# Optimization experiments

Measured on AMD Instinct MI355X. Metric: run time of the kernel, lower is better.

Reference implementation:

```python
import jax, jax.numpy as jnp
import numpy as np

CLIP_FRAMES = 16
CLIP_STRIDE = 8
D_CODE = 256
K_CODE = 8192
ENC_DIM = 128 * CLIP_FRAMES * 4 * 4  # 32768
EPS = 1e-5


def setup_inputs() -> dict:
    key = jax.random.key(0)
    ks = jax.random.split(key, 16)
    rn = lambda k, s, sc: (jax.random.normal(k, s, jnp.float32) * sc)
    inp = {}
    inp['x'] = jax.random.normal(ks[0], (4, 3, 64, 96, 96), jnp.float32)
    inp['conv1_w'] = rn(ks[1], (32, 3, 3, 3, 3), 0.1)
    inp['conv1_b'] = jnp.zeros((32,), jnp.float32)
    inp['bn1_g'] = jnp.ones((32,), jnp.float32)
    inp['bn1_b'] = jnp.zeros((32,), jnp.float32)
    inp['conv2_w'] = rn(ks[2], (64, 32, 3, 3, 3), 0.05)
    inp['conv2_b'] = jnp.zeros((64,), jnp.float32)
    inp['bn2_g'] = jnp.ones((64,), jnp.float32)
    inp['bn2_b'] = jnp.zeros((64,), jnp.float32)
    inp['conv3_w'] = rn(ks[3], (128, 64, 3, 3, 3), 0.04)
    inp['conv3_b'] = jnp.zeros((128,), jnp.float32)
    inp['bn3_g'] = jnp.ones((128,), jnp.float32)
    inp['bn3_b'] = jnp.zeros((128,), jnp.float32)
    inp['proj_w'] = rn(ks[4], (D_CODE, ENC_DIM), 0.005)
    inp['proj_b'] = jnp.zeros((D_CODE,), jnp.float32)
    inp['codebook'] = jax.random.uniform(ks[5], (K_CODE, D_CODE), jnp.float32, -1.0 / K_CODE, 1.0 / K_CODE)
    inp['gru_w_ih'] = rn(ks[6], (3 * D_CODE, D_CODE), 0.05)
    inp['gru_w_hh'] = rn(ks[7], (3 * D_CODE, D_CODE), 0.05)
    inp['gru_b_ih'] = jnp.zeros((3 * D_CODE,), jnp.float32)
    inp['gru_b_hh'] = jnp.zeros((3 * D_CODE,), jnp.float32)
    return inp


def _conv3d(x, w, b):
    y = jax.lax.conv_general_dilated(x, w, (1, 1, 1), ((1, 1), (1, 1), (1, 1)),
                                     dimension_numbers=('NCDHW', 'OIDHW', 'NCDHW'))
    return y + b[None, :, None, None, None]


def _bn(x, g, b):
    # training-mode BatchNorm3d: batch stats over (N,D,H,W), biased variance
    m = x.mean(axis=(0, 2, 3, 4), keepdims=True)
    v = ((x - m) ** 2).mean(axis=(0, 2, 3, 4), keepdims=True)
    return g[None, :, None, None, None] * (x - m) * jax.lax.rsqrt(v + EPS) + b[None, :, None, None, None]


def _maxpool(x):
    return jax.lax.reduce_window(x, -jnp.inf, jax.lax.max, (1, 1, 1, 2, 2), (1, 1, 1, 2, 2), 'VALID')


def _adaptive_avgpool(x):
    # [N,128,16,24,24] -> [N,128,16,4,4]; 24/4=6 exact window
    s = jax.lax.reduce_window(x, 0.0, jax.lax.add, (1, 1, 1, 6, 6), (1, 1, 1, 6, 6), 'VALID')
    return s / 36.0


def _gru(xs, w_ih, w_hh, b_ih, b_hh):
    # torch GRU, batch_first, h0=0. xs: [B,L,D]
    B, L, D = xs.shape
    gx = jnp.einsum('bld,gd->blg', xs, w_ih) + b_ih  # [B,L,3D]

    def step(h, gx_t):
        gh = h @ w_hh.T + b_hh
        xr, xz, xn = jnp.split(gx_t, 3, axis=-1)
        hr, hz, hn = jnp.split(gh, 3, axis=-1)
        r = jax.nn.sigmoid(xr + hr)
        z = jax.nn.sigmoid(xz + hz)
        n = jnp.tanh(xn + r * hn)
        h2 = (1.0 - z) * n + z * h
        return h2, h2

    h0 = jnp.zeros((B, D), xs.dtype)
    _, ys = jax.lax.scan(step, h0, jnp.swapaxes(gx, 0, 1))
    return jnp.swapaxes(ys, 0, 1)  # [B,L,D]


def _forward(x, conv1_w, conv1_b, bn1_g, bn1_b, conv2_w, conv2_b, bn2_g, bn2_b,
             conv3_w, conv3_b, bn3_g, bn3_b, proj_w, proj_b, codebook,
             gru_w_ih, gru_w_hh, gru_b_ih, gru_b_hh):
    B, C, T, H, W = x.shape
    num_clips = max(1, (T - CLIP_FRAMES) // CLIP_STRIDE + 1)
    clips = jnp.stack([x[:, :, i * CLIP_STRIDE:i * CLIP_STRIDE + CLIP_FRAMES] for i in range(num_clips)])

    def encode(clip):  # clip: [B,3,16,96,96]; BN stats per-clip like the torch loop
        h = jax.nn.relu(_bn(_conv3d(clip, conv1_w, conv1_b), bn1_g, bn1_b))
        h = _maxpool(h)
        h = jax.nn.relu(_bn(_conv3d(h, conv2_w, conv2_b), bn2_g, bn2_b))
        h = _maxpool(h)
        h = jax.nn.relu(_bn(_conv3d(h, conv3_w, conv3_b), bn3_g, bn3_b))
        h = _adaptive_avgpool(h)            # [B,128,16,4,4]
        h = h.reshape(B, -1)                # [B, 32768]
        return h @ proj_w.T + proj_b        # [B, D_CODE]

    features = jnp.swapaxes(jax.vmap(encode)(clips), 0, 1)  # [B,L,D]
    L, D = features.shape[1], features.shape[2]

    # quantize: squared-Euclidean argmin (same argmin as torch.cdist p=2)
    flat = features.reshape(-1, D)
    d2 = (flat * flat).sum(-1, keepdims=True) - 2.0 * flat @ codebook.T + (codebook * codebook).sum(-1)
    token_indices = jnp.argmin(d2, axis=-1)
    quantized = codebook[token_indices].reshape(B, L, D)

    sg = jax.lax.stop_gradient
    commitment_loss = jnp.mean((features - sg(quantized)) ** 2)
    codebook_loss = jnp.mean((quantized - sg(features)) ** 2)
    context_features = _gru(quantized[:, :-1], gru_w_ih, gru_w_hh, gru_b_ih, gru_b_hh)
    context_loss = jnp.mean((context_features - features[:, 1:]) ** 2)
    vq_loss = commitment_loss + 0.25 * codebook_loss + 0.1 * context_loss
    return token_indices.reshape(B, L), quantized, commitment_loss, codebook_loss, context_loss, vq_loss


def reference(x, conv1_w, conv1_b, bn1_g, bn1_b, conv2_w, conv2_b, bn2_g, bn2_b,
              conv3_w, conv3_b, bn3_g, bn3_b, proj_w, proj_b, codebook,
              gru_w_ih, gru_w_hh, gru_b_ih, gru_b_hh):
    return _forward(x, conv1_w, conv1_b, bn1_g, bn1_b, conv2_w, conv2_b, bn2_g, bn2_b,
                    conv3_w, conv3_b, bn3_g, bn3_b, proj_w, proj_b, codebook,
                    gru_w_ih, gru_w_hh, gru_b_ih, gru_b_hh)
```

## Files before the change

### kernel.cpp

```cpp
#include <hip/hip_runtime.h>
#include <math.h>


typedef __attribute__((ext_vector_type(8))) short short8;
typedef __attribute__((ext_vector_type(4))) float f32x4;

__device__ inline unsigned short f2bf(float x) {
    unsigned int u = __float_as_uint(x);
    u += 0x7FFFu + ((u >> 16) & 1u);
    return (unsigned short)(u >> 16);
}
__device__ inline float bf2f(unsigned short h) {
    return __uint_as_float(((unsigned int)h) << 16);
}
__device__ inline f32x4 vmax4(f32x4 a, f32x4 b) {
    return (f32x4){fmaxf(a.x, b.x), fmaxf(a.y, b.y), fmaxf(a.z, b.z), fmaxf(a.w, b.w)};
}
__device__ inline f32x4 vmin4(f32x4 a, f32x4 b) {
    return (f32x4){fminf(a.x, b.x), fminf(a.y, b.y), fminf(a.z, b.z), fminf(a.w, b.w)};
}

#define C1LOADR(J) \
    f32x4 u = *(const f32x4*)(ip + (J) * 36); \
    f32x4 w4 = *(const f32x4*)(ip + (J) * 36 + 4); \
    f32x4 sA = u; \
    f32x4 sB = __builtin_shufflevector(u, w4, 1, 2, 3, 4); \
    f32x4 sC = __builtin_shufflevector(u, w4, 2, 3, 4, 5);
#define C1UPD0(I) a0_##I += wa0 * sA + wa1 * sB + wa2 * sC; a1_##I += wb0 * sA + wb1 * sB + wb2 * sC;
#define C1UPD1(I) a0_##I += wa3 * sA + wa4 * sB + wa5 * sC; a1_##I += wb3 * sA + wb4 * sB + wb5 * sC;
#define C1UPD2(I) a0_##I += wa6 * sA + wa7 * sB + wa8 * sC; a1_##I += wb6 * sA + wb7 * sB + wb8 * sC;

__launch_bounds__(256, 3)
__global__ void conv1k(const float* __restrict__ x, const float* __restrict__ wgt,
                       const float* __restrict__ bias, float* __restrict__ pmax,
                       float* __restrict__ pmin, float* __restrict__ stats, int t0) {
    int bb = blockIdx.x;
    int xt = bb % 3; int yt = (bb / 3) % 4; int t = (bb / 12) % 16; int n = bb / 192;
    int x0 = xt * 32, y0 = yt * 24;
    __shared__ float tile[9 * 936];
    __shared__ float wl[3456];
    __shared__ float sst[64];
    int tid = threadIdx.x;
    for (int i = tid; i < 3456; i += 256) {
        int idx = i % 12; int r = i / 12;
        int co = r & 31; int p = r >> 5;
        wl[i] = idx < 9 ? wgt[co * 81 + p * 9 + idx] : 0.f;
    }
    if (tid < 64) sst[tid] = 0.f;
    for (int i = tid; i < 7956; i += 256) {
        int p = i / 884; int rem = i % 884;
        int r = rem / 34, cl = rem % 34;
        int ci = p / 3, kt = p % 3;
        int lt = t + kt - 1;
        int yy = y0 + r - 1, xx = x0 + cl - 1;
        float v = 0.f;
        if (lt >= 0 && lt <= 15 && yy >= 0 && yy < 96 && xx >= 0 && xx < 96)
            v = x[((size_t)(n * 3 + ci) * 64 + (t0 + lt)) * 9216 + yy * 96 + cl + x0 - 1];
        tile[p * 936 + r * 36 + cl] = v;
    }
    __syncthreads();

    int cg = tid & 15;
    int co0 = cg * 2;
    float bv0 = bias[co0], bv1 = bias[co0 + 1];
    float ls0 = 0.f, lq0 = 0.f, ls1 = 0.f, lq1 = 0.f;
    size_t nt48 = (size_t)(n * 16 + t) * 48;

    #pragma unroll 1
    for (int rr = 0; rr < 3; ++rr) {
        int sp = rr * 16 + (tid >> 4);
        int tx = sp & 7, ty = sp >> 3;
        f32x4 a0_0 = (f32x4)bv0, a0_1 = (f32x4)bv0, a0_2 = (f32x4)bv0, a0_3 = (f32x4)bv0;
        f32x4 a1_0 = (f32x4)bv1, a1_1 = (f32x4)bv1, a1_2 = (f32x4)bv1, a1_3 = (f32x4)bv1;

        #pragma unroll 1
        for (int p = 0; p < 9; ++p) {
            const float* wpk = wl + ((p * 32 + co0) * 12);
            f32x4 wv0 = *(const f32x4*)(wpk);
            f32x4 wv1 = *(const f32x4*)(wpk + 4);
            f32x4 wv2 = *(const f32x4*)(wpk + 8);
            f32x4 wv3 = *(const f32x4*)(wpk + 12);
            f32x4 wv4 = *(const f32x4*)(wpk + 16);
            f32x4 wv5 = *(const f32x4*)(wpk + 20);
            float wa0 = wv0.x, wa1 = wv0.y, wa2 = wv0.z, wa3 = wv0.w;
            float wa4 = wv1.x, wa5 = wv1.y, wa6 = wv1.z, wa7 = wv1.w;
            float wa8 = wv2.x;
            float wb0 = wv3.x, wb1 = wv3.y, wb2 = wv3.z, wb3 = wv3.w;
            float wb4 = wv4.x, wb5 = wv4.y, wb6 = wv4.z, wb7 = wv4.w;
            float wb8 = wv5.x;
            const float* ip = tile + p * 936 + (ty * 4) * 36 + tx * 4;
            { C1LOADR(0) C1UPD0(0) }
            { C1LOADR(1) C1UPD0(1) C1UPD1(0) }
            { C1LOADR(2) C1UPD0(2) C1UPD1(1) C1UPD2(0) }
            { C1LOADR(3) C1UPD0(3) C1UPD1(2) C1UPD2(1) }
            { C1LOADR(4) C1UPD1(3) C1UPD2(2) }
            { C1LOADR(5) C1UPD2(3) }
        }

        f32x4 s4 = a0_0 + a0_1 + a0_2 + a0_3;
        ls0 += s4.x + s4.y + s4.z + s4.w;
        f32x4 q4 = a0_0 * a0_0 + a0_1 * a0_1 + a0_2 * a0_2 + a0_3 * a0_3;
        lq0 += q4.x + q4.y + q4.z + q4.w;
        f32x4 s5 = a1_0 + a1_1 + a1_2 + a1_3;
        ls1 += s5.x + s5.y + s5.z + s5.w;
        f32x4 q5 = a1_0 * a1_0 + a1_1 * a1_1 + a1_2 * a1_2 + a1_3 * a1_3;
        lq1 += q5.x + q5.y + q5.z + q5.w;

        f32x4 mx0a = vmax4(a0_0, a0_1), mx0b = vmax4(a0_2, a0_3);
        f32x4 mn0a = vmin4(a0_0, a0_1), mn0b = vmin4(a0_2, a0_3);
        f32x4 mx1a = vmax4(a1_0, a1_1), mx1b = vmax4(a1_2, a1_3);
        f32x4 mn1a = vmin4(a1_0, a1_1), mn1b = vmin4(a1_2, a1_3);
        size_t row0 = (nt48 + (size_t)(yt * 12 + ty * 2)) * 1536 + (size_t)(xt * 16 + tx * 2) * 32 + co0;
        size_t row1 = row0 + 1536;
        *(float2*)(pmax + row0)      = make_float2(fmaxf(mx0a.x, mx0a.y), fmaxf(mx1a.x, mx1a.y));
        *(float2*)(pmax + row0 + 32) = make_float2(fmaxf(mx0a.z, mx0a.w), fmaxf(mx1a.z, mx1a.w));
        *(float2*)(pmax + row1)      = make_float2(fmaxf(mx0b.x, mx0b.y), fmaxf(mx1b.x, mx1b.y));
        *(float2*)(pmax + row1 + 32) = make_float2(fmaxf(mx0b.z, mx0b.w), fmaxf(mx1b.z, mx1b.w));
        *(float2*)(pmin + row0)      = make_float2(fminf(mn0a.x, mn0a.y), fminf(mn1a.x, mn1a.y));
        *(float2*)(pmin + row0 + 32) = make_float2(fminf(mn0a.z, mn0a.w), fminf(mn1a.z, mn1a.w));
        *(float2*)(pmin + row1)      = make_float2(fminf(mn0b.x, mn0b.y), fminf(mn1b.x, mn1b.y));
        *(float2*)(pmin + row1 + 32) = make_float2(fminf(mn0b.z, mn0b.w), fminf(mn1b.z, mn1b.w));
    }

    ls0 += __shfl_xor(ls0, 16, 64); ls0 += __shfl_xor(ls0, 32, 64);
    lq0 += __shfl_xor(lq0, 16, 64); lq0 += __shfl_xor(lq0, 32, 64);
    ls1 += __shfl_xor(ls1, 16, 64); ls1 += __shfl_xor(ls1, 32, 64);
    lq1 += __shfl_xor(lq1, 16, 64); lq1 += __shfl_xor(lq1, 32, 64);
    if ((tid & 63) < 16) {
        atomicAdd(&sst[co0 * 2], ls0);
        atomicAdd(&sst[co0 * 2 + 1], lq0);
        atomicAdd(&sst[co0 * 2 + 2], ls1);
        atomicAdd(&sst[co0 * 2 + 3], lq1);
    }
    __syncthreads();
    if (tid < 64) atomicAdd(&stats[tid], sst[tid]);
}

__global__ void bnpool1b(const float* __restrict__ pmax, const float* __restrict__ pmin,
                         const float* __restrict__ st, const float* __restrict__ gam,
                         const float* __restrict__ bet,
                         unsigned short* __restrict__ phi, unsigned short* __restrict__ plo) {
    int i = blockIdx.x * 256 + threadIdx.x;
    int c8 = i & 3; int xo = (i >> 2) % 48; int yo = (i / 192) % 48;
    int t = (i / 9216) % 16; int n = i / 147456;
    size_t base = (((size_t)(n * 16 + t) * 48 + yo) * 48 + xo) * 32 + c8 * 8;
    union { unsigned short s[8]; uint4 v; } Uh, Ul;
    #pragma unroll
    for (int j = 0; j < 8; ++j) {
        int ch = c8 * 8 + j;
        float mean = st[ch * 2] * (1.f / 589824.f);
        float var  = st[ch * 2 + 1] * (1.f / 589824.f) - mean * mean;
        var = var < 0.f ? 0.f : var;
        float sc = gam[ch] / sqrtf(var + 1e-5f);
        float sh = bet[ch] - mean * sc;
        float pv = sc >= 0.f ? pmax[base + j] : pmin[base + j];
        float v = fmaxf(sc * pv + sh, 0.f);
        Uh.s[j] = f2bf(v);
        Ul.s[j] = f2bf(v - bf2f(Uh.s[j]));
    }
    size_t off = ((((size_t)n * 18 + t + 1) * 50 + yo + 1) * 52 + (xo + 1)) * 32 + c8 * 8;
    *(uint4*)(phi + off) = Uh.v;
    *(uint4*)(plo + off) = Ul.v;
}

__launch_bounds__(256, 4)
__global__ void conv2k(const unsigned short* __restrict__ phi, const unsigned short* __restrict__ plo,
                       const unsigned short* __restrict__ w2p, const float* __restrict__ bias,
                       float* __restrict__ out, float* __restrict__ st) {
    __shared__ unsigned short tin[2 * 6 * 52 * 32];
    float (*sred)[64] = (float (*)[64])(tin);
    float (*qred)[64] = (float (*)[64])(tin + 512);
    int b = blockIdx.x;
    int y0 = (b % 12) * 4; int t = (b / 12) % 16; int n = b / 192;
    int wv = threadIdx.x >> 6, lane = threadIdx.x & 63;
    int c = lane & 15, q = lane >> 4;
    int y = y0 + wv;

    f32x4 acc[4][3];
    #pragma unroll
    for (int i = 0; i < 4; ++i)
        #pragma unroll
        for (int j = 0; j < 3; ++j) acc[i][j] = (f32x4)0.f;

    for (int kt = 0; kt < 3; ++kt) {
        const unsigned short* srch = phi + (size_t)(n * 18 + t + kt) * (50 * 52 * 32);
        const unsigned short* srcl = plo + (size_t)(n * 18 + t + kt) * (50 * 52 * 32);
        __syncthreads();
        for (int i = threadIdx.x; i < 2496; i += 256) {
            int g = i & 3; int xx = (i >> 2) % 52; int rh = (i >> 2) / 52;
            int row = rh % 6; int h = rh / 6;
            int sg = g ^ (xx & 3) ^ ((xx >> 2) & 3);
            const unsigned short* src = (h ? srcl : srch) + (size_t)(y0 + row) * 1664 + xx * 32 + g * 8;
            *(uint4*)(tin + ((rh * 52 + xx) << 5) + (sg << 3)) = *(const uint4*)src;
        }
        __syncthreads();
        const unsigned short* wkt = w2p + kt * 36864 + c * 32 + q * 8;
        #pragma unroll 1
        for (int ky = 0; ky < 3; ++ky) {
            int row = wv + ky;
            #pragma unroll
            for (int kx = 0; kx < 3; ++kx) {
                const unsigned short* wb = wkt + (ky * 3 + kx) * 4096;
                short8 ah[4], al[4], bh[3], bl[3];
                #pragma unroll
                for (int mb = 0; mb < 4; ++mb) {
                    ah[mb] = *(const short8*)(wb + mb * 512);
                    al[mb] = *(const short8*)(wb + 2048 + mb * 512);
                }
                #pragma unroll
                for (int xt = 0; xt < 3; ++xt) {
                    int xx = xt * 16 + kx + c;
                    int sq = (q ^ (xx & 3) ^ ((xx >> 2) & 3)) << 3;
                    bh[xt] = *(const short8*)(tin + ((row * 52 + xx) << 5) + sq);
                    bl[xt] = *(const short8*)(tin + (((6 + row) * 52 + xx) << 5) + sq);
                }
                #pragma unroll
                for (int mb = 0; mb < 4; ++mb)
                    #pragma unroll
                    for (int xt = 0; xt < 3; ++xt) {
                        acc[mb][xt] = __builtin_amdgcn_mfma_f32_16x16x32_bf16(ah[mb], bh[xt], acc[mb][xt], 0, 0, 0);
                        acc[mb][xt] = __builtin_amdgcn_mfma_f32_16x16x32_bf16(ah[mb], bl[xt], acc[mb][xt], 0, 0, 0);
                        acc[mb][xt] = __builtin_amdgcn_mfma_f32_16x16x32_bf16(al[mb], bh[xt], acc[mb][xt], 0, 0, 0);
                    }
            }
        }
    }
    __syncthreads();
    float* ob = out + (((size_t)(n * 16 + t) * 48) + y) * (48 * 64);
    #pragma unroll
    for (int mb = 0; mb < 4; ++mb) {
        f32x4 bv = *(const f32x4*)(bias + mb * 16 + q * 4);
        f32x4 v0 = acc[mb][0] + bv, v1 = acc[mb][1] + bv, v2 = acc[mb][2] + bv;
        *(f32x4*)(ob + (0 * 16 + c) * 64 + mb * 16 + q * 4) = v0;
        *(f32x4*)(ob + (1 * 16 + c) * 64 + mb * 16 + q * 4) = v1;
        *(f32x4*)(ob + (2 * 16 + c) * 64 + mb * 16 + q * 4) = v2;
        #pragma unroll
        for (int r = 0; r < 4; ++r) {
            float s  = v0[r] + v1[r] + v2[r];
            float q2 = v0[r] * v0[r] + v1[r] * v1[r] + v2[r] * v2[r];
            #pragma unroll
            for (int m = 1; m < 16; m <<= 1) { s += __shfl_xor(s, m, 64); q2 += __shfl_xor(q2, m, 64); }
            if (c == 0) { sred[wv][mb * 16 + q * 4 + r] = s; qred[wv][mb * 16 + q * 4 + r] = q2; }
        }
    }
    __syncthreads();
    if (threadIdx.x < 64) {
        float s = sred[0][threadIdx.x] + sred[1][threadIdx.x] + sred[2][threadIdx.x] + sred[3][threadIdx.x];
        float q2 = qred[0][threadIdx.x] + qred[1][threadIdx.x] + qred[2][threadIdx.x] + qred[3][threadIdx.x];
        atomicAdd(&st[threadIdx.x * 2], s);
        atomicAdd(&st[threadIdx.x * 2 + 1], q2);
    }
}

__global__ void bnpool2k(const float* __restrict__ cin, const float* __restrict__ st,
                         const float* __restrict__ gam, const float* __restrict__ bet,
                         unsigned short* __restrict__ phi, unsigned short* __restrict__ plo) {
    int i = blockIdx.x * 256 + threadIdx.x;
    if (i >= 509184) return;
    int oc = i & 7; int xp = (i >> 3) % 34; int yp = (i / 272) % 26;
    int tp = (i / 7072) % 18; int n = i / 127296;
    union { unsigned short s[8]; uint4 v; } Uh, Ul;
    if (tp >= 1 && tp <= 16 && yp >= 1 && yp <= 24 && xp >= 1 && xp <= 24) {
        int t = tp - 1, yo = yp - 1, xo = xp - 1;
        const float* b0 = cin + ((((size_t)(n * 16 + t) * 48) + 2 * yo) * 48 + 2 * xo) * 64 + oc * 8;
        #pragma unroll
        for (int j = 0; j < 8; ++j) {
            int ch = oc * 8 + j;
            float mean = st[ch * 2] * (1.f / 147456.f);
            float var  = st[ch * 2 + 1] * (1.f / 147456.f) - mean * mean;
            var = var < 0.f ? 0.f : var;
            float sc = gam[ch] / sqrtf(var + 1e-5f);
            float sh = bet[ch] - mean * sc;
            float a  = b0[j] * sc + sh;
            float bb = b0[64 + j] * sc + sh;
            float c2 = b0[3072 + j] * sc + sh;
            float d  = b0[3136 + j] * sc + sh;
            float v = fmaxf(fmaxf(fmaxf(a, bb), fmaxf(c2, d)), 0.f);
            Uh.s[j] = f2bf(v);
            Ul.s[j] = f2bf(v - bf2f(Uh.s[j]));
        }
    } else {
        Uh.v = make_uint4(0, 0, 0, 0);
        Ul.v = make_uint4(0, 0, 0, 0);
    }
    size_t off = ((((size_t)n * 18 + tp) * 26 + yp) * 34 + xp) * 64 + oc * 8;
    *(uint4*)(phi + off) = Uh.v;
    *(uint4*)(plo + off) = Ul.v;
}

__launch_bounds__(256, 3)
__global__ void conv3k(const unsigned short* __restrict__ phi, const unsigned short* __restrict__ plo,
                       const unsigned short* __restrict__ w3p, const float* __restrict__ bias,
                       float* __restrict__ out, float* __restrict__ st) {
    __shared__ unsigned short tin[2 * 6 * 34 * 64];
    float (*sred)[64] = (float (*)[64])(tin);
    float (*qred)[64] = (float (*)[64])(tin + 512);
    int b = blockIdx.x;
    int y0 = (b % 6) * 4; int t = (b / 6) % 16; int n = (b / 96) % 4; int cg = b / 384;
    int wv = threadIdx.x >> 6, lane = threadIdx.x & 63;
    int c = lane & 15, q = lane >> 4;
    int y = y0 + wv;

    f32x4 acc[4][2];
    #pragma unroll
    for (int i = 0; i < 4; ++i) { acc[i][0] = (f32x4)0.f; acc[i][1] = (f32x4)0.f; }

    const unsigned short* wsrc = w3p + (size_t)cg * 221184 + c * 32 + q * 8;

    for (int kt = 0; kt < 3; ++kt) {
        const unsigned short* srch = phi + (size_t)(n * 18 + t + kt) * (26 * 34 * 64);
        const unsigned short* srcl = plo + (size_t)(n * 18 + t + kt) * (26 * 34 * 64);
        __syncthreads();
        for (int i = threadIdx.x; i < 3264; i += 256) {
            int g = i & 7; int xx = (i >> 3) % 34; int rh = (i >> 3) / 34;
            int row = rh % 6; int h = rh / 6;
            const unsigned short* src = (h ? srcl : srch) + (size_t)(y0 + row) * 2176 + xx * 64 + g * 8;
            *(uint4*)(tin + ((rh * 34 + xx) << 6) + ((g ^ (xx & 7)) << 3)) = *(const uint4*)src;
        }
        __syncthreads();
        const unsigned short* wkt = wsrc + kt * 73728;
        #pragma unroll 1
        for (int ky = 0; ky < 3; ++ky) {
            int row = wv + ky;
            const unsigned short* wky = wkt + ky * 24576;
            #pragma unroll
            for (int kx = 0; kx < 3; ++kx) {
                #pragma unroll
                for (int kc = 0; kc < 2; ++kc) {
                    const unsigned short* wb = wky + kx * 8192 + kc * 2048;
                    short8 ah[4], al[4], bh[2], bl[2];
                    #pragma unroll
                    for (int mb = 0; mb < 4; ++mb) {
                        ah[mb] = *(const short8*)(wb + mb * 512);
                        al[mb] = *(const short8*)(wb + 4096 + mb * 512);
                    }
                    #pragma unroll
                    for (int xt = 0; xt < 2; ++xt) {
                        int xx = xt * 16 + kx + c;
                        int so = ((kc * 4 + q) ^ (xx & 7)) << 3;
                        bh[xt] = *(const short8*)(tin + ((row * 34 + xx) << 6) + so);
                        bl[xt] = *(const short8*)(tin + (((6 + row) * 34 + xx) << 6) + so);
                    }
                    #pragma unroll
                    for (int mb = 0; mb < 4; ++mb)
                        #pragma unroll
                        for (int xt = 0; xt < 2; ++xt) {
                            acc[mb][xt] = __builtin_amdgcn_mfma_f32_16x16x32_bf16(ah[mb], bh[xt], acc[mb][xt], 0, 0, 0);
                            acc[mb][xt] = __builtin_amdgcn_mfma_f32_16x16x32_bf16(ah[mb], bl[xt], acc[mb][xt], 0, 0, 0);
                            acc[mb][xt] = __builtin_amdgcn_mfma_f32_16x16x32_bf16(al[mb], bh[xt], acc[mb][xt], 0, 0, 0);
                        }
                }
            }
        }
    }
    __syncthreads();
    float* ob = out + (((size_t)(n * 16 + t) * 24) + y) * (24 * 128) + cg * 64;
    #pragma unroll
    for (int mb = 0; mb < 4; ++mb) {
        f32x4 bv = *(const f32x4*)(bias + cg * 64 + mb * 16 + q * 4);
        f32x4 v0 = acc[mb][0] + bv;
        f32x4 v1 = acc[mb][1] + bv;
        *(f32x4*)(ob + c * 128 + mb * 16 + q * 4) = v0;
        if (c < 8) *(f32x4*)(ob + (16 + c) * 128 + mb * 16 + q * 4) = v1;
        #pragma unroll
        for (int r = 0; r < 4; ++r) {
            float s  = v0[r] + (c < 8 ? v1[r] : 0.f);
            float q2 = v0[r] * v0[r] + (c < 8 ? v1[r] * v1[r] : 0.f);
            #pragma unroll
            for (int m = 1; m < 16; m <<= 1) { s += __shfl_xor(s, m, 64); q2 += __shfl_xor(q2, m, 64); }
            if (c == 0) { sred[wv][mb * 16 + q * 4 + r] = s; qred[wv][mb * 16 + q * 4 + r] = q2; }
        }
    }
    __syncthreads();
    if (threadIdx.x < 64) {
        int co = cg * 64 + threadIdx.x;
        float s = sred[0][threadIdx.x] + sred[1][threadIdx.x] + sred[2][threadIdx.x] + sred[3][threadIdx.x];
        float q2 = qred[0][threadIdx.x] + qred[1][threadIdx.x] + qred[2][threadIdx.x] + qred[3][threadIdx.x];
        atomicAdd(&st[co * 2], s);
        atomicAdd(&st[co * 2 + 1], q2);
    }
}

__global__ void bnavgk(const float* __restrict__ x, const float* __restrict__ st,
                       const float* __restrict__ gam, const float* __restrict__ bet,
                       float* __restrict__ enc) {
    int i = blockIdx.x * 256 + threadIdx.x;
    int c = i & 127; int xo = (i >> 7) & 3; int yo = (i >> 9) & 3;
    int t = (i >> 11) & 15; int n = i >> 15;
    float mean = st[c * 2] * (1.f / 36864.f);
    float var  = st[c * 2 + 1] * (1.f / 36864.f) - mean * mean;
    var = var < 0.f ? 0.f : var;
    float sc = gam[c] / sqrtf(var + 1e-5f);
    float sh = bet[c] - mean * sc;
    const float* base = x + ((((size_t)(n * 16 + t) * 24) + yo * 6) * 24 + xo * 6) * 128 + c;
    float s = 0.f;
    #pragma unroll
    for (int wy = 0; wy < 6; ++wy)
        #pragma unroll
        for (int wx = 0; wx < 6; ++wx)
            s += fmaxf(base[(wy * 24 + wx) * 128] * sc + sh, 0.f);
    enc[(size_t)n * 32768 + (size_t)c * 256 + t * 16 + yo * 4 + xo] = s * (1.f / 36.f);
}

__global__ void prep2k(const float* __restrict__ c2w, unsigned short* __restrict__ w2p) {
    int i = blockIdx.x * 256 + threadIdx.x;
    if (i >= 110592) return;
    int ci = i & 31; int co = (i >> 5) & 63; int h = (i >> 11) & 1;
    int o = (i >> 12) % 9; int kt = i / 36864;
    int ky = o / 3, kx = o % 3;
    float w = c2w[(((size_t)(co * 32 + ci) * 3 + kt) * 3 + ky) * 3 + kx];
    unsigned short hi = f2bf(w);
    w2p[i] = h ? f2bf(w - bf2f(hi)) : hi;
}
__global__ void prep3k(const float* __restrict__ c3w, unsigned short* __restrict__ w3p) {
    int i = blockIdx.x * 256 + threadIdx.x;
    if (i >= 442368) return;
    int cil = i & 31; int cop = (i >> 5) & 63; int kc = (i >> 11) & 1; int h = (i >> 12) & 1;
    int kx = (i >> 13) % 3; int ky = (i / 24576) % 3; int kt = (i / 73728) % 3; int cg = i / 221184;
    int ci = kc * 32 + cil; int co = cg * 64 + cop;
    float w = c3w[(((size_t)(co * 64 + ci) * 3 + kt) * 3 + ky) * 3 + kx];
    unsigned short hi = f2bf(w);
    w3p[i] = h ? f2bf(w - bf2f(hi)) : hi;
}
__global__ void prepwhhk(const float* __restrict__ whh, float* __restrict__ wt) {
    int i = blockIdx.x * 256 + threadIdx.x;
    int g = i % 768, k = i / 768;
    wt[i] = whh[(size_t)g * 256 + k];
}

__global__ void transck(const float* __restrict__ cb, float* __restrict__ cbT) {
    __shared__ float t[32][33];
    int bx = blockIdx.x & 255;
    int by = blockIdx.x >> 8;
    int ld = threadIdx.x & 31, lk = threadIdx.x >> 5;
    #pragma unroll
    for (int i = 0; i < 4; ++i) {
        int kl = lk + i * 8;
        t[kl][ld] = cb[(size_t)(bx * 32 + kl) * 256 + by * 32 + ld];
    }
    __syncthreads();
    #pragma unroll
    for (int i = 0; i < 4; ++i) {
        int dl = lk + i * 8;
        cbT[(size_t)(by * 32 + dl) * 8192 + bx * 32 + ld] = t[ld][dl];
    }
}

__global__ void cnormk(const float* __restrict__ cbT, double* __restrict__ cn2) {
    int k = blockIdx.x * 256 + threadIdx.x;
    double s = 0.0;
    for (int d = 0; d < 256; ++d) {
        double c = (double)cbT[(size_t)d * 8192 + k];
        s += c * c;
    }
    cn2[k] = s;
}

__global__ void projinitk(const float* __restrict__ pb, float* __restrict__ feat) {
    int i = blockIdx.x * 256 + threadIdx.x;
    feat[i] = pb[i & 255];
}

__global__ void projk(const float* __restrict__ enc, const float* __restrict__ pw,
                      float* __restrict__ feat) {
    int d = blockIdx.x & 255; int ch = blockIdx.x >> 8;
    int k0 = ch * 4096;
    float acc[28];
    #pragma unroll
    for (int e = 0; e < 28; ++e) acc[e] = 0.f;
    const float* wrow = pw + (size_t)d * 32768 + k0;
    for (int k = threadIdx.x; k < 4096; k += 256) {
        float wv = wrow[k];
        #pragma unroll
        for (int e = 0; e < 28; ++e) acc[e] += enc[(size_t)e * 32768 + k0 + k] * wv;
    }
    __shared__ float red[4 * 28];
    #pragma unroll
    for (int e = 0; e < 28; ++e) {
        float v = acc[e];
        #pragma unroll
        for (int o = 32; o > 0; o >>= 1) v += __shfl_down(v, o, 64);
        if ((threadIdx.x & 63) == 0) red[(threadIdx.x >> 6) * 28 + e] = v;
    }
    __syncthreads();
    if (threadIdx.x < 28) {
        int e = threadIdx.x;
        int l = e >> 2, n = e & 3;
        float s = red[e] + red[28 + e] + red[56 + e] + red[84 + e];
        atomicAdd(&feat[(size_t)(n * 7 + l) * 256 + d], s);
    }
}

__global__ void quantk(const float* __restrict__ feat, const float* __restrict__ cbT,
                       const double* __restrict__ cn2, unsigned long long* __restrict__ best) {
    int kc = blockIdx.x & 31, r = blockIdx.x >> 5;
    int k = kc * 256 + threadIdx.x;
    __shared__ float fs[256];
    fs[threadIdx.x] = feat[(size_t)r * 256 + threadIdx.x];
    __syncthreads();
    double dot = 0.0;
    for (int d = 0; d < 256; ++d)
        dot += (double)cbT[(size_t)d * 8192 + k] * (double)fs[d];
    float s = (float)(cn2[k] - 2.0 * dot);
    unsigned int bits = __float_as_uint(s);
    unsigned int key = (bits & 0x80000000u) ? ~bits : (bits | 0x80000000u);
    unsigned long long p = ((unsigned long long)key << 32) | (unsigned int)k;
// ... 159 lines not shown
```

Measured before the change: 2.377 ms.

## Double-buffer conv2/conv3 weight fragments in registers and remap block indices

Fully unrolls the ky/kx(/kc) loops in conv2k and conv3k and ping-pongs weight fragment loads between two register sets (P/Q), so the global weight loads for the next tap are issued while the MFMAs for the current tap run. The first weight fragment is also fetched before the shared-memory tile fill to hide its latency. Block index decoding is changed so that consecutive blocks interleave batch and time-half, which alters L2 locality and how work spreads across XCDs. conv2k's launch bound drops from 4 to 3 waves to leave room for the extra registers, risking lower occupancy.

Result: faster. 2.305 ms (-3.0%).

```diff
diff --git a/kernel.cpp b/kernel.cpp
--- a/kernel.cpp
+++ b/kernel.cpp
@@ -19,6 +19,8 @@
 __device__ inline f32x4 vmin4(f32x4 a, f32x4 b) {
     return (f32x4){fminf(a.x, b.x), fminf(a.y, b.y), fminf(a.z, b.z), fminf(a.w, b.w)};
 }
+
+#define MF(d, a, b) d = __builtin_amdgcn_mfma_f32_16x16x32_bf16(a, b, d, 0, 0, 0)
 
 #define C1LOADR(J) \
     f32x4 u = *(const f32x4*)(ip + (J) * 36); \
@@ -163,7 +165,43 @@
     *(uint4*)(plo + off) = Ul.v;
 }
 
-__launch_bounds__(256, 4)
+#define DECLW(S) short8 S##a0, S##a1, S##a2, S##a3, S##l0, S##l1, S##l2, S##l3;
+
+#define LOADW2(S, KY, KX) { \
+    const unsigned short* wb_ = wkt + ((KY) * 3 + (KX)) * 4096; \
+    S##a0 = *(const short8*)(wb_);        S##a1 = *(const short8*)(wb_ + 512); \
+    S##a2 = *(const short8*)(wb_ + 1024); S##a3 = *(const short8*)(wb_ + 1536); \
+    S##l0 = *(const short8*)(wb_ + 2048); S##l1 = *(const short8*)(wb_ + 2560); \
+    S##l2 = *(const short8*)(wb_ + 3072); S##l3 = *(const short8*)(wb_ + 3584); \
+}
+
+#define COMPUTE2(S, KY, KX) { \
+    int row_ = wv + (KY); \
+    int xx0_ = (KX) + c, xx1_ = 16 + (KX) + c, xx2_ = 32 + (KX) + c; \
+    int sq0_ = (q ^ (xx0_ & 3) ^ ((xx0_ >> 2) & 3)) << 3; \
+    int sq1_ = (q ^ (xx1_ & 3) ^ ((xx1_ >> 2) & 3)) << 3; \
+    int sq2_ = (q ^ (xx2_ & 3) ^ ((xx2_ >> 2) & 3)) << 3; \
+    short8 bh0_ = *(const short8*)(tin + ((row_ * 52 + xx0_) << 5) + sq0_); \
+    short8 bl0_ = *(const short8*)(tin + (((6 + row_) * 52 + xx0_) << 5) + sq0_); \
+    short8 bh1_ = *(const short8*)(tin + ((row_ * 52 + xx1_) << 5) + sq1_); \
+    short8 bl1_ = *(const short8*)(tin + (((6 + row_) * 52 + xx1_) << 5) + sq1_); \
+    short8 bh2_ = *(const short8*)(tin + ((row_ * 52 + xx2_) << 5) + sq2_); \
+    short8 bl2_ = *(const short8*)(tin + (((6 + row_) * 52 + xx2_) << 5) + sq2_); \
+    MF(acc[0][0], S##a0, bh0_); MF(acc[0][0], S##a0, bl0_); MF(acc[0][0], S##l0, bh0_); \
+    MF(acc[0][1], S##a0, bh1_); MF(acc[0][1], S##a0, bl1_); MF(acc[0][1], S##l0, bh1_); \
+    MF(acc[0][2], S##a0, bh2_); MF(acc[0][2], S##a0, bl2_); MF(acc[0][2], S##l0, bh2_); \
+    MF(acc[1][0], S##a1, bh0_); MF(acc[1][0], S##a1, bl0_); MF(acc[1][0], S##l1, bh0_); \
+    MF(acc[1][1], S##a1, bh1_); MF(acc[1][1], S##a1, bl1_); MF(acc[1][1], S##l1, bh1_); \
+    MF(acc[1][2], S##a1, bh2_); MF(acc[1][2], S##a1, bl2_); MF(acc[1][2], S##l1, bh2_); \
+    MF(acc[2][0], S##a2, bh0_); MF(acc[2][0], S##a2, bl0_); MF(acc[2][0], S##l2, bh0_); \
+    MF(acc[2][1], S##a2, bh1_); MF(acc[2][1], S##a2, bl1_); MF(acc[2][1], S##l2, bh1_); \
+    MF(acc[2][2], S##a2, bh2_); MF(acc[2][2], S##a2, bl2_); MF(acc[2][2], S##l2, bh2_); \
+    MF(acc[3][0], S##a3, bh0_); MF(acc[3][0], S##a3, bl0_); MF(acc[3][0], S##l3, bh0_); \
+    MF(acc[3][1], S##a3, bh1_); MF(acc[3][1], S##a3, bl1_); MF(acc[3][1], S##l3, bh1_); \
+    MF(acc[3][2], S##a3, bh2_); MF(acc[3][2], S##a3, bl2_); MF(acc[3][2], S##l3, bh2_); \
+}
+
+__launch_bounds__(256, 3)
 __global__ void conv2k(const unsigned short* __restrict__ phi, const unsigned short* __restrict__ plo,
                        const unsigned short* __restrict__ w2p, const float* __restrict__ bias,
                        float* __restrict__ out, float* __restrict__ st) {
@@ -171,7 +209,10 @@
     float (*sred)[64] = (float (*)[64])(tin);
     float (*qred)[64] = (float (*)[64])(tin + 512);
     int b = blockIdx.x;
-    int y0 = (b % 12) * 4; int t = (b / 12) % 16; int n = b / 192;
+    int k8 = b & 7, i96 = b >> 3;
+    int n = k8 >> 1, th = k8 & 1;
+    int tt = i96 / 12; int y0 = (i96 - tt * 12) * 4;
+    int t = th * 8 + tt;
     int wv = threadIdx.x >> 6, lane = threadIdx.x & 63;
     int c = lane & 15, q = lane >> 4;
     int y = y0 + wv;
@@ -182,9 +223,14 @@
         #pragma unroll
         for (int j = 0; j < 3; ++j) acc[i][j] = (f32x4)0.f;
 
+    DECLW(P) DECLW(Q)
+
+    #pragma unroll 1
     for (int kt = 0; kt < 3; ++kt) {
         const unsigned short* srch = phi + (size_t)(n * 18 + t + kt) * (50 * 52 * 32);
         const unsigned short* srcl = plo + (size_t)(n * 18 + t + kt) * (50 * 52 * 32);
+        const unsigned short* wkt = w2p + kt * 36864 + c * 32 + q * 8;
+        LOADW2(P, 0, 0)
         __syncthreads();
         for (int i = threadIdx.x; i < 2496; i += 256) {
             int g = i & 3; int xx = (i >> 2) % 52; int rh = (i >> 2) / 52;
@@ -194,36 +240,15 @@
             *(uint4*)(tin + ((rh * 52 + xx) << 5) + (sg << 3)) = *(const uint4*)src;
         }
         __syncthreads();
-        const unsigned short* wkt = w2p + kt * 36864 + c * 32 + q * 8;
-        #pragma unroll 1
-        for (int ky = 0; ky < 3; ++ky) {
-            int row = wv + ky;
-            #pragma unroll
-            for (int kx = 0; kx < 3; ++kx) {
-                const unsigned short* wb = wkt + (ky * 3 + kx) * 4096;
-                short8 ah[4], al[4], bh[3], bl[3];
-                #pragma unroll
-                for (int mb = 0; mb < 4; ++mb) {
-                    ah[mb] = *(const short8*)(wb + mb * 512);
-                    al[mb] = *(const short8*)(wb + 2048 + mb * 512);
-                }
-                #pragma unroll
-                for (int xt = 0; xt < 3; ++xt) {
-                    int xx = xt * 16 + kx + c;
-                    int sq = (q ^ (xx & 3) ^ ((xx >> 2) & 3)) << 3;
-                    bh[xt] = *(const short8*)(tin + ((row * 52 + xx) << 5) + sq);
-                    bl[xt] = *(const short8*)(tin + (((6 + row) * 52 + xx) << 5) + sq);
-                }
-                #pragma unroll
-                for (int mb = 0; mb < 4; ++mb)
-                    #pragma unroll
-                    for (int xt = 0; xt < 3; ++xt) {
-                        acc[mb][xt] = __builtin_amdgcn_mfma_f32_16x16x32_bf16(ah[mb], bh[xt], acc[mb][xt], 0, 0, 0);
-                        acc[mb][xt] = __builtin_amdgcn_mfma_f32_16x16x32_bf16(ah[mb], bl[xt], acc[mb][xt], 0, 0, 0);
-                        acc[mb][xt] = __builtin_amdgcn_mfma_f32_16x16x32_bf16(al[mb], bh[xt], acc[mb][xt], 0, 0, 0);
-                    }
-            }
-        }
+        LOADW2(Q, 0, 1) COMPUTE2(P, 0, 0)
+        LOADW2(P, 0, 2) COMPUTE2(Q, 0, 1)
+        LOADW2(Q, 1, 0) COMPUTE2(P, 0, 2)
+        LOADW2(P, 1, 1) COMPUTE2(Q, 1, 0)
+        LOADW2(Q, 1, 2) COMPUTE2(P, 1, 1)
+        LOADW2(P, 2, 0) COMPUTE2(Q, 1, 2)
+        LOADW2(Q, 2, 1) COMPUTE2(P, 2, 0)
+        LOADW2(P, 2, 2) COMPUTE2(Q, 2, 1)
+        COMPUTE2(P, 2, 2)
     }
     __syncthreads();
     float* ob = out + (((size_t)(n * 16 + t) * 48) + y) * (48 * 64);
@@ -288,6 +313,33 @@
     *(uint4*)(plo + off) = Ul.v;
 }
 
+#define LOADW3(S, KY, KX, KC) { \
+    const unsigned short* wb_ = wkt + (KY) * 24576 + (KX) * 8192 + (KC) * 2048; \
+    S##a0 = *(const short8*)(wb_);        S##a1 = *(const short8*)(wb_ + 512); \
+    S##a2 = *(const short8*)(wb_ + 1024); S##a3 = *(const short8*)(wb_ + 1536); \
+    S##l0 = *(const short8*)(wb_ + 4096); S##l1 = *(const short8*)(wb_ + 4608); \
+    S##l2 = *(const short8*)(wb_ + 5120); S##l3 = *(const short8*)(wb_ + 5632); \
+}
+
+#define COMPUTE3(S, KY, KX, KC) { \
+    int row_ = wv + (KY); \
+    int xx0_ = (KX) + c, xx1_ = 16 + (KX) + c; \
+    int so0_ = (((KC) * 4 + q) ^ (xx0_ & 7)) << 3; \
+    int so1_ = (((KC) * 4 + q) ^ (xx1_ & 7)) << 3; \
+    short8 bh0_ = *(const short8*)(tin + ((row_ * 34 + xx0_) << 6) + so0_); \
+    short8 bl0_ = *(const short8*)(tin + (((6 + row_) * 34 + xx0_) << 6) + so0_); \
+    short8 bh1_ = *(const short8*)(tin + ((row_ * 34 + xx1_) << 6) + so1_); \
+    short8 bl1_ = *(const short8*)(tin + (((6 + row_) * 34 + xx1_) << 6) + so1_); \
+    MF(acc[0][0], S##a0, bh0_); MF(acc[0][0], S##a0, bl0_); MF(acc[0][0], S##l0, bh0_); \
+    MF(acc[0][1], S##a0, bh1_); MF(acc[0][1], S##a0, bl1_); MF(acc[0][1], S##l0, bh1_); \
+    MF(acc[1][0], S##a1, bh0_); MF(acc[1][0], S##a1, bl0_); MF(acc[1][0], S##l1, bh0_); \
+    MF(acc[1][1], S##a1, bh1_); MF(acc[1][1], S##a1, bl1_); MF(acc[1][1], S##l1, bh1_); \
+    MF(acc[2][0], S##a2, bh0_); MF(acc[2][0], S##a2, bl0_); MF(acc[2][0], S##l2, bh0_); \
+    MF(acc[2][1], S##a2, bh1_); MF(acc[2][1], S##a2, bl1_); MF(acc[2][1], S##l2, bh1_); \
+    MF(acc[3][0], S##a3, bh0_); MF(acc[3][0], S##a3, bl0_); MF(acc[3][0], S##l3, bh0_); \
+    MF(acc[3][1], S##a3, bh1_); MF(acc[3][1], S##a3, bl1_); MF(acc[3][1], S##l3, bh1_); \
+}
+
 __launch_bounds__(256, 3)
 __global__ void conv3k(const unsigned short* __restrict__ phi, const unsigned short* __restrict__ plo,
                        const unsigned short* __restrict__ w3p, const float* __restrict__ bias,
@@ -296,7 +348,11 @@
     float (*sred)[64] = (float (*)[64])(tin);
     float (*qred)[64] = (float (*)[64])(tin + 512);
     int b = blockIdx.x;
-    int y0 = (b % 6) * 4; int t = (b / 6) % 16; int n = (b / 96) % 4; int cg = b / 384;
+    int k8 = b & 7, i96 = b >> 3;
+    int n = k8 >> 1, th = k8 & 1;
+    int cg = i96 / 48; int r48 = i96 - cg * 48;
+    int tt = r48 / 6;  int y0 = (r48 - tt * 6) * 4;
+    int t = th * 8 + tt;
     int wv = threadIdx.x >> 6, lane = threadIdx.x & 63;
     int c = lane & 15, q = lane >> 4;
     int y = y0 + wv;
@@ -306,10 +362,14 @@
     for (int i = 0; i < 4; ++i) { acc[i][0] = (f32x4)0.f; acc[i][1] = (f32x4)0.f; }
 
     const unsigned short* wsrc = w3p + (size_t)cg * 221184 + c * 32 + q * 8;
-
+    DECLW(P) DECLW(Q)
+
+    #pragma unroll 1
     for (int kt = 0; kt < 3; ++kt) {
         const unsigned short* srch = phi + (size_t)(n * 18 + t + kt) * (26 * 34 * 64);
         const unsigned short* srcl = plo + (size_t)(n * 18 + t + kt) * (26 * 34 * 64);
+        const unsigned short* wkt = wsrc + kt * 73728;
+        LOADW3(P, 0, 0, 0)
         __syncthreads();
         for (int i = threadIdx.x; i < 3264; i += 256) {
             int g = i & 7; int xx = (i >> 3) % 34; int rh = (i >> 3) / 34;
@@ -318,40 +378,24 @@
             *(uint4*)(tin + ((rh * 34 + xx) << 6) + ((g ^ (xx & 7)) << 3)) = *(const uint4*)src;
         }
         __syncthreads();
-        const unsigned short* wkt = wsrc + kt * 73728;
-        #pragma unroll 1
-        for (int ky = 0; ky < 3; ++ky) {
-            int row = wv + ky;
-            const unsigned short* wky = wkt + ky * 24576;
-            #pragma unroll
-            for (int kx = 0; kx < 3; ++kx) {
-                #pragma unroll
-                for (int kc = 0; kc < 2; ++kc) {
-                    const unsigned short* wb = wky + kx * 8192 + kc * 2048;
-                    short8 ah[4], al[4], bh[2], bl[2];
-                    #pragma unroll
-                    for (int mb = 0; mb < 4; ++mb) {
-                        ah[mb] = *(const short8*)(wb + mb * 512);
-                        al[mb] = *(const short8*)(wb + 4096 + mb * 512);
-                    }
-                    #pragma unroll
-                    for (int xt = 0; xt < 2; ++xt) {
-                        int xx = xt * 16 + kx + c;
-                        int so = ((kc * 4 + q) ^ (xx & 7)) << 3;
-                        bh[xt] = *(const short8*)(tin + ((row * 34 + xx) << 6) + so);
-                        bl[xt] = *(const short8*)(tin + (((6 + row) * 34 + xx) << 6) + so);
-                    }
-                    #pragma unroll
-                    for (int mb = 0; mb < 4; ++mb)
-                        #pragma unroll
-                        for (int xt = 0; xt < 2; ++xt) {
-                            acc[mb][xt] = __builtin_amdgcn_mfma_f32_16x16x32_bf16(ah[mb], bh[xt], acc[mb][xt], 0, 0, 0);
-                            acc[mb][xt] = __builtin_amdgcn_mfma_f32_16x16x32_bf16(ah[mb], bl[xt], acc[mb][xt], 0, 0, 0);
-                            acc[mb][xt] = __builtin_amdgcn_mfma_f32_16x16x32_bf16(al[mb], bh[xt], acc[mb][xt], 0, 0, 0);
-                        }
-                }
-            }
-        }
+        LOADW3(Q, 0, 0, 1) COMPUTE3(P, 0, 0, 0)
+        LOADW3(P, 0, 1, 0) COMPUTE3(Q, 0, 0, 1)
+        LOADW3(Q, 0, 1, 1) COMPUTE3(P, 0, 1, 0)
+        LOADW3(P, 0, 2, 0) COMPUTE3(Q, 0, 1, 1)
+        LOADW3(Q, 0, 2, 1) COMPUTE3(P, 0, 2, 0)
+        LOADW3(P, 1, 0, 0) COMPUTE3(Q, 0, 2, 1)
+        LOADW3(Q, 1, 0, 1) COMPUTE3(P, 1, 0, 0)
+        LOADW3(P, 1, 1, 0) COMPUTE3(Q, 1, 0, 1)
+        LOADW3(Q, 1, 1, 1) COMPUTE3(P, 1, 1, 0)
+        LOADW3(P, 1, 2, 0) COMPUTE3(Q, 1, 1, 1)
+        LOADW3(Q, 1, 2, 1) COMPUTE3(P, 1, 2, 0)
+        LOADW3(P, 2, 0, 0) COMPUTE3(Q, 1, 2, 1)
+        LOADW3(Q, 2, 0, 1) COMPUTE3(P, 2, 0, 0)
+        LOADW3(P, 2, 1, 0) COMPUTE3(Q, 2, 0, 1)
+        LOADW3(Q, 2, 1, 1) COMPUTE3(P, 2, 1, 0)
+        LOADW3(P, 2, 2, 0) COMPUTE3(Q, 2, 1, 1)
+        LOADW3(Q, 2, 2, 1) COMPUTE3(P, 2, 2, 0)
+        COMPUTE3(Q, 2, 2, 1)
     }
     __syncthreads();
     float* ob = out + (((size_t)(n * 16 + t) * 24) + y) * (24 * 128) + cg * 64;
```

## Pad LDS tiles instead of XOR swizzle, remap blocks, unroll ky in conv2/conv3

Applied to the files above, without the earlier changes.

Conv2 and conv3 now store input tiles in LDS with padded row strides (40 and 72 shorts) instead of an XOR swizzle. Tile pointers are precomputed so the inner loop uses constant offsets and no per-iteration index math. The ky loop is fully unrolled, conv3 loads only the 26 x-columns it needs (with clamped addresses for the second x-tile), and block indices are remapped so that n and the time half vary fastest across neighbouring blocks. Conv2's launch bound drops to 3 waves per SIMD, which gives each thread more registers but lowers possible occupancy.

Measured after the change: 2.323 ms. 2.3% less time.

```diff
diff --git a/kernel.cpp b/kernel.cpp
--- a/kernel.cpp
+++ b/kernel.cpp
@@ -19,6 +19,8 @@
 __device__ inline f32x4 vmin4(f32x4 a, f32x4 b) {
     return (f32x4){fminf(a.x, b.x), fminf(a.y, b.y), fminf(a.z, b.z), fminf(a.w, b.w)};
 }
+
+#define MF(d, a, b) d = __builtin_amdgcn_mfma_f32_16x16x32_bf16(a, b, d, 0, 0, 0)
 
 #define C1LOADR(J) \
     f32x4 u = *(const f32x4*)(ip + (J) * 36); \
@@ -163,15 +165,18 @@
     *(uint4*)(plo + off) = Ul.v;
 }
 
-__launch_bounds__(256, 4)
+__launch_bounds__(256, 3)
 __global__ void conv2k(const unsigned short* __restrict__ phi, const unsigned short* __restrict__ plo,
                        const unsigned short* __restrict__ w2p, const float* __restrict__ bias,
                        float* __restrict__ out, float* __restrict__ st) {
-    __shared__ unsigned short tin[2 * 6 * 52 * 32];
+    __shared__ unsigned short tin[12 * 52 * 40];
     float (*sred)[64] = (float (*)[64])(tin);
     float (*qred)[64] = (float (*)[64])(tin + 512);
     int b = blockIdx.x;
-    int y0 = (b % 12) * 4; int t = (b / 12) % 16; int n = b / 192;
+    int k8 = b & 7, i96 = b >> 3;
+    int n = k8 >> 1, th = k8 & 1;
+    int tt = i96 / 12; int y0 = (i96 - tt * 12) * 4;
+    int t = th * 8 + tt;
     int wv = threadIdx.x >> 6, lane = threadIdx.x & 63;
     int c = lane & 15, q = lane >> 4;
     int y = y0 + wv;
@@ -182,45 +187,49 @@
         #pragma unroll
         for (int j = 0; j < 3; ++j) acc[i][j] = (f32x4)0.f;
 
+    const int loff = c * 32 + q * 8;
+    const unsigned short* tb0 = tin + (wv * 52 + c) * 40 + q * 8;
+    const unsigned short* tb1 = tb0 + 16 * 40;
+    const unsigned short* tb2 = tb0 + 32 * 40;
+
+    #pragma unroll 1
     for (int kt = 0; kt < 3; ++kt) {
         const unsigned short* srch = phi + (size_t)(n * 18 + t + kt) * (50 * 52 * 32);
         const unsigned short* srcl = plo + (size_t)(n * 18 + t + kt) * (50 * 52 * 32);
+        const unsigned short* wkt = w2p + kt * 36864;
         __syncthreads();
         for (int i = threadIdx.x; i < 2496; i += 256) {
             int g = i & 3; int xx = (i >> 2) % 52; int rh = (i >> 2) / 52;
             int row = rh % 6; int h = rh / 6;
-            int sg = g ^ (xx & 3) ^ ((xx >> 2) & 3);
             const unsigned short* src = (h ? srcl : srch) + (size_t)(y0 + row) * 1664 + xx * 32 + g * 8;
-            *(uint4*)(tin + ((rh * 52 + xx) << 5) + (sg << 3)) = *(const uint4*)src;
+            *(uint4*)(tin + (rh * 52 + xx) * 40 + (g << 3)) = *(const uint4*)src;
         }
         __syncthreads();
-        const unsigned short* wkt = w2p + kt * 36864 + c * 32 + q * 8;
-        #pragma unroll 1
+        #pragma unroll
         for (int ky = 0; ky < 3; ++ky) {
-            int row = wv + ky;
             #pragma unroll
             for (int kx = 0; kx < 3; ++kx) {
                 const unsigned short* wb = wkt + (ky * 3 + kx) * 4096;
                 short8 ah[4], al[4], bh[3], bl[3];
                 #pragma unroll
                 for (int mb = 0; mb < 4; ++mb) {
-                    ah[mb] = *(const short8*)(wb + mb * 512);
-                    al[mb] = *(const short8*)(wb + 2048 + mb * 512);
+                    ah[mb] = *(const short8*)(wb + loff + mb * 512);
+                    al[mb] = *(const short8*)(wb + 2048 + loff + mb * 512);
                 }
-                #pragma unroll
-                for (int xt = 0; xt < 3; ++xt) {
-                    int xx = xt * 16 + kx + c;
-                    int sq = (q ^ (xx & 3) ^ ((xx >> 2) & 3)) << 3;
-                    bh[xt] = *(const short8*)(tin + ((row * 52 + xx) << 5) + sq);
-                    bl[xt] = *(const short8*)(tin + (((6 + row) * 52 + xx) << 5) + sq);
-                }
+                int off = (ky * 52 + kx) * 40;
+                bh[0] = *(const short8*)(tb0 + off);
+                bl[0] = *(const short8*)(tb0 + off + 12480);
+                bh[1] = *(const short8*)(tb1 + off);
+                bl[1] = *(const short8*)(tb1 + off + 12480);
+                bh[2] = *(const short8*)(tb2 + off);
+                bl[2] = *(const short8*)(tb2 + off + 12480);
                 #pragma unroll
                 for (int mb = 0; mb < 4; ++mb)
                     #pragma unroll
                     for (int xt = 0; xt < 3; ++xt) {
-                        acc[mb][xt] = __builtin_amdgcn_mfma_f32_16x16x32_bf16(ah[mb], bh[xt], acc[mb][xt], 0, 0, 0);
-                        acc[mb][xt] = __builtin_amdgcn_mfma_f32_16x16x32_bf16(ah[mb], bl[xt], acc[mb][xt], 0, 0, 0);
-                        acc[mb][xt] = __builtin_amdgcn_mfma_f32_16x16x32_bf16(al[mb], bh[xt], acc[mb][xt], 0, 0, 0);
+                        MF(acc[mb][xt], ah[mb], bh[xt]);
+                        MF(acc[mb][xt], ah[mb], bl[xt]);
+                        MF(acc[mb][xt], al[mb], bh[xt]);
                     }
             }
         }
@@ -292,11 +301,15 @@
 __global__ void conv3k(const unsigned short* __restrict__ phi, const unsigned short* __restrict__ plo,
                        const unsigned short* __restrict__ w3p, const float* __restrict__ bias,
                        float* __restrict__ out, float* __restrict__ st) {
-    __shared__ unsigned short tin[2 * 6 * 34 * 64];
+    __shared__ unsigned short tin[12 * 26 * 72];
     float (*sred)[64] = (float (*)[64])(tin);
     float (*qred)[64] = (float (*)[64])(tin + 512);
     int b = blockIdx.x;
-    int y0 = (b % 6) * 4; int t = (b / 6) % 16; int n = (b / 96) % 4; int cg = b / 384;
+    int k8 = b & 7, i96 = b >> 3;
+    int n = k8 >> 1, th = k8 & 1;
+    int cg = i96 / 48; int r48 = i96 - cg * 48;
+    int tt = r48 / 6;  int y0 = (r48 - tt * 6) * 4;
+    int t = th * 8 + tt;
     int wv = threadIdx.x >> 6, lane = threadIdx.x & 63;
     int c = lane & 15, q = lane >> 4;
     int y = y0 + wv;
@@ -305,49 +318,56 @@
     #pragma unroll
     for (int i = 0; i < 4; ++i) { acc[i][0] = (f32x4)0.f; acc[i][1] = (f32x4)0.f; }
 
-    const unsigned short* wsrc = w3p + (size_t)cg * 221184 + c * 32 + q * 8;
-
+    const int loff = c * 32 + q * 8;
+    const unsigned short* wkt0 = w3p + (size_t)cg * 221184;
+    const unsigned short* vb0 = tin + (wv * 26 + c) * 72 + q * 8;
+    int x10 = 16 + 0 + c; x10 = x10 > 25 ? 25 : x10;
+    int x11 = 16 + 1 + c; x11 = x11 > 25 ? 25 : x11;
+    int x12 = 16 + 2 + c; x12 = x12 > 25 ? 25 : x12;
+    const unsigned short* vb1_0 = tin + (wv * 26 + x10) * 72 + q * 8;
+    const unsigned short* vb1_1 = tin + (wv * 26 + x11) * 72 + q * 8;
+    const unsigned short* vb1_2 = tin + (wv * 26 + x12) * 72 + q * 8;
+
+    #pragma unroll 1
     for (int kt = 0; kt < 3; ++kt) {
         const unsigned short* srch = phi + (size_t)(n * 18 + t + kt) * (26 * 34 * 64);
         const unsigned short* srcl = plo + (size_t)(n * 18 + t + kt) * (26 * 34 * 64);
+        const unsigned short* wkt = wkt0 + kt * 73728;
         __syncthreads();
-        for (int i = threadIdx.x; i < 3264; i += 256) {
-            int g = i & 7; int xx = (i >> 3) % 34; int rh = (i >> 3) / 34;
+        for (int i = threadIdx.x; i < 2496; i += 256) {
+            int g = i & 7; int xx = (i >> 3) % 26; int rh = (i >> 3) / 26;
             int row = rh % 6; int h = rh / 6;
             const unsigned short* src = (h ? srcl : srch) + (size_t)(y0 + row) * 2176 + xx * 64 + g * 8;
-            *(uint4*)(tin + ((rh * 34 + xx) << 6) + ((g ^ (xx & 7)) << 3)) = *(const uint4*)src;
+            *(uint4*)(tin + (rh * 26 + xx) * 72 + (g << 3)) = *(const uint4*)src;
         }
         __syncthreads();
-        const unsigned short* wkt = wsrc + kt * 73728;
-        #pragma unroll 1
+        #pragma unroll
         for (int ky = 0; ky < 3; ++ky) {
-            int row = wv + ky;
-            const unsigned short* wky = wkt + ky * 24576;
             #pragma unroll
             for (int kx = 0; kx < 3; ++kx) {
                 #pragma unroll
                 for (int kc = 0; kc < 2; ++kc) {
-                    const unsigned short* wb = wky + kx * 8192 + kc * 2048;
+                    const unsigned short* wb = wkt + ky * 24576 + kx * 8192 + kc * 2048;
                     short8 ah[4], al[4], bh[2], bl[2];
                     #pragma unroll
                     for (int mb = 0; mb < 4; ++mb) {
-                        ah[mb] = *(const short8*)(wb + mb * 512);
-                        al[mb] = *(const short8*)(wb + 4096 + mb * 512);
+                        ah[mb] = *(const short8*)(wb + loff + mb * 512);
+                        al[mb] = *(const short8*)(wb + 4096 + loff + mb * 512);
                     }
-                    #pragma unroll
-                    for (int xt = 0; xt < 2; ++xt) {
-                        int xx = xt * 16 + kx + c;
-                        int so = ((kc * 4 + q) ^ (xx & 7)) << 3;
-                        bh[xt] = *(const short8*)(tin + ((row * 34 + xx) << 6) + so);
-                        bl[xt] = *(const short8*)(tin + (((6 + row) * 34 + xx) << 6) + so);
-                    }
+                    int off0 = ky * 1872 + kx * 72 + kc * 32;
+                    int off1 = ky * 1872 + kc * 32;
+                    const unsigned short* vb1 = (kx == 0) ? vb1_0 : (kx == 1) ? vb1_1 : vb1_2;
+                    bh[0] = *(const short8*)(vb0 + off0);
+                    bl[0] = *(const short8*)(vb0 + off0 + 11232);
+                    bh[1] = *(const short8*)(vb1 + off1);
+                    bl[1] = *(const short8*)(vb1 + off1 + 11232);
                     #pragma unroll
                     for (int mb = 0; mb < 4; ++mb)
                         #pragma unroll
                         for (int xt = 0; xt < 2; ++xt) {
-                            acc[mb][xt] = __builtin_amdgcn_mfma_f32_16x16x32_bf16(ah[mb], bh[xt], acc[mb][xt], 0, 0, 0);
-                            acc[mb][xt] = __builtin_amdgcn_mfma_f32_16x16x32_bf16(ah[mb], bl[xt], acc[mb][xt], 0, 0, 0);
-                            acc[mb][xt] = __builtin_amdgcn_mfma_f32_16x16x32_bf16(al[mb], bh[xt], acc[mb][xt], 0, 0, 0);
+                            MF(acc[mb][xt], ah[mb], bh[xt]);
+                            MF(acc[mb][xt], ah[mb], bl[xt]);
+                            MF(acc[mb][xt], al[mb], bh[xt]);
                         }
                 }
             }
```
